# Performance work log

Measured on AMD Instinct MI355X. Metric: run time of the kernel, lower is better.

The kernel has to match this reference:

```python
import jax, jax.numpy as jnp
import numpy as np

N_NODES = 50000
N_EDGES = 1600000
IN_DIM = 128
HID = 64
HEADS = 4
N_GRAPHS = 64
OUT_DIM = 10
NEG_SLOPE = 0.2  # PyG GATConv default leaky_relu slope


def _glorot(key, shape):
    fan_in = shape[0] if len(shape) > 1 else shape[-1]
    return jax.random.normal(key, shape, dtype=jnp.float32) / np.sqrt(fan_in)


def setup_inputs() -> dict:
    key = jax.random.key(0)
    ks = jax.random.split(key, 24)
    imgs = jax.random.normal(ks[0], (N_NODES, IN_DIM), dtype=jnp.float32)
    edge_index = jax.random.randint(ks[1], (2, N_EDGES), 0, N_NODES, dtype=jnp.int32)
    batch = jnp.sort(jax.random.randint(ks[2], (N_NODES,), 0, N_GRAPHS, dtype=jnp.int32))
    HC = HID * HEADS
    inp = {
        'imgs': imgs, 'edge_index': edge_index, 'batch': batch,
        # superpixel aggregator: Linear(input_dim, hidden)
        'W_agg': _glorot(ks[3], (IN_DIM, HID)), 'b_agg': jnp.zeros((HID,), jnp.float32),
        # GAT layer 0: hidden -> heads*hidden, concat
        'W0': _glorot(ks[4], (HID, HC)), 'as0': _glorot(ks[5], (HEADS, HID)), 'ad0': _glorot(ks[6], (HEADS, HID)), 'b0': jnp.zeros((HC,), jnp.float32),
        # GAT layer 1: heads*hidden -> heads*hidden, concat
        'W1': _glorot(ks[7], (HC, HC)), 'as1': _glorot(ks[8], (HEADS, HID)), 'ad1': _glorot(ks[9], (HEADS, HID)), 'b1': jnp.zeros((HC,), jnp.float32),
        # GAT layer 2: heads*hidden -> hidden, mean over heads
        'W2': _glorot(ks[10], (HC, HC)), 'as2': _glorot(ks[11], (HEADS, HID)), 'ad2': _glorot(ks[12], (HEADS, HID)), 'b2': jnp.zeros((HID,), jnp.float32),
        # MLP: hidden -> hidden -> out
        'mW1': _glorot(ks[13], (HID, HID)), 'mb1': jnp.zeros((HID,), jnp.float32),
        'mW2': _glorot(ks[14], (HID, OUT_DIM)), 'mb2': jnp.zeros((OUT_DIM,), jnp.float32),
    }
    return inp


def _gat_conv(x, src, dst, W, a_src, a_dst, b, concat):
    # PyG GATConv: linear -> per-head scores -> leaky_relu -> segment softmax over dst -> scatter-add
    N = x.shape[0]
    H, C = a_src.shape
    h = (x @ W).reshape(N, H, C)                      # [N,H,C]
    es = jnp.sum(h * a_src, axis=-1)                  # [N,H]
    ed = jnp.sum(h * a_dst, axis=-1)                  # [N,H]
    e = jax.nn.leaky_relu(es[src] + ed[dst], NEG_SLOPE)  # [E,H]
    m = jax.ops.segment_max(e, dst, num_segments=N)
    m = jnp.where(jnp.isfinite(m), m, 0.0)
    ex = jnp.exp(e - m[dst])                          # [E,H]
    s = jax.ops.segment_sum(ex, dst, num_segments=N)
    alpha = ex / (s[dst] + 1e-16)                     # [E,H]
    out = jax.ops.segment_sum(h[src] * alpha[..., None], dst, num_segments=N)  # [N,H,C]
    out = out.reshape(N, H * C) if concat else out.mean(axis=1)
    return out + b


def _forward(imgs, edge_index, batch, W_agg, b_agg, W0, as0, ad0, b0, W1, as1, ad1, b1, W2, as2, ad2, b2, mW1, mb1, mW2, mb2):
    N = imgs.shape[0]
    # add self loops (PyG GATConv default add_self_loops=True)
    loop = jnp.arange(N, dtype=edge_index.dtype)
    src = jnp.concatenate([edge_index[0], loop])
    dst = jnp.concatenate([edge_index[1], loop])
    x = imgs @ W_agg + b_agg                          # lrgb aggregator
    x = jax.nn.elu(_gat_conv(x, src, dst, W0, as0, ad0, b0, True))
    x = jax.nn.elu(_gat_conv(x, src, dst, W1, as1, ad1, b1, True))
    x = _gat_conv(x, src, dst, W2, as2, ad2, b2, False)
    # global mean pool over graphs
    sums = jax.ops.segment_sum(x, batch, num_segments=N_GRAPHS)
    cnt = jax.ops.segment_sum(jnp.ones((N,), x.dtype), batch, num_segments=N_GRAPHS)
    pooled = sums / jnp.maximum(cnt, 1.0)[:, None]
    # MLP (dropout inactive at inference)
    hmlp = jax.nn.relu(pooled @ mW1 + mb1)
    return hmlp @ mW2 + mb2


def reference(imgs, edge_index, batch, W_agg, b_agg, W0, as0, ad0, b0, W1, as1, ad1, b1, W2, as2, ad2, b2, mW1, mb1, mW2, mb2):
    return _forward(imgs, edge_index, batch, W_agg, b_agg, W0, as0, ad0, b0, W1, as1, ad1, b1, W2, as2, ad2, b2, mW1, mb1, mW2, mb2)
```

## Files before the change

### kernel.cpp

```cpp
#include <hip/hip_runtime.h>
#include <hip/hip_bf16.h>

#define N_NODES 50000
#define N_EDGESX 1600000
#define E_TOT   (N_EDGESX + N_NODES)
#define IN_DIM 128
#define HID 64
#define HEADS 4
#define HC 256
#define N_GRAPHS 64
#define OUT_DIM 10
#define NEG_SLOPE 0.2f

#define NBUK 196
#define CAP 12288
#define BT 4096

typedef __attribute__((ext_vector_type(8))) short bf16x8;
typedef __attribute__((ext_vector_type(4))) float f32x4;

__device__ __forceinline__ float lrelu(float x){ return fmaxf(x, NEG_SLOPE*x); }
__device__ __forceinline__ float sel4(float4 v, int i){
  float r = v.x;
  r = (i==1) ? v.y : r;
  r = (i==2) ? v.z : r;
  r = (i==3) ? v.w : r;
  return r;
}
__device__ __forceinline__ unsigned short f2bf(float f){
  union { __hip_bfloat16 b; unsigned short u; } cv;
  cv.b = __float2bfloat16(f);
  return cv.u;
}
__device__ __forceinline__ float bf2f(unsigned short u){ return __uint_as_float(((unsigned)u) << 16); }
__device__ __forceinline__ float bflo(unsigned int u){ return __uint_as_float(u << 16); }
__device__ __forceinline__ float bfhi(unsigned int u){ return __uint_as_float(u & 0xffff0000u); }

__global__ __launch_bounds__(256) void bin_k(const int* __restrict__ ei,
                                             int* __restrict__ bucket_cursor,
                                             unsigned int* __restrict__ bucket_buf){
  __shared__ unsigned int pk[BT];
  __shared__ unsigned int binned[BT];
  __shared__ int hist[256], excl[256], gbase[256], lcur[256], tmp[256];
  const int tid = threadIdx.x;
  const int e0 = blockIdx.x * BT;
  const int nv = min(BT, E_TOT - e0);
  hist[tid] = 0;
  __syncthreads();
  for (int i = tid; i < nv; i += 256){
    int e = e0 + i;
    int src, dst;
    if (e < N_EDGESX){ src = ei[e]; dst = ei[N_EDGESX + e]; }
    else { src = e - N_EDGESX; dst = src; }
    pk[i] = ((unsigned)src << 16) | (unsigned)dst;
    atomicAdd(&hist[dst >> 8], 1);
  }
  __syncthreads();
  int v = hist[tid];
  tmp[tid] = v;
  __syncthreads();
  for (int off = 1; off < 256; off <<= 1){
    int t = (tid >= off) ? tmp[tid-off] : 0;
    __syncthreads();
    tmp[tid] += t;
    __syncthreads();
  }
  excl[tid] = tmp[tid] - v;
  lcur[tid] = tmp[tid] - v;
  if (tid < NBUK && v > 0) gbase[tid] = atomicAdd(&bucket_cursor[tid], v);
  __syncthreads();
  for (int i = tid; i < nv; i += 256){
    unsigned u = pk[i];
    int b = (int)((u & 0xFFFFu) >> 8);
    int p = atomicAdd(&lcur[b], 1);
    binned[p] = u;
  }
  __syncthreads();
  for (int j = tid; j < nv; j += 256){
    unsigned u = binned[j];
    int b = (int)((u & 0xFFFFu) >> 8);
    bucket_buf[(size_t)b*CAP + gbase[b] + (j - excl[b])] = u;
  }
}

__global__ __launch_bounds__(256) void bucket_scan_k(const int* __restrict__ bucket_cursor,
                                                     int* __restrict__ bucket_base,
                                                     int* __restrict__ row_start){
  __shared__ int tmp[256];
  int t = threadIdx.x;
  int v = (t < NBUK) ? bucket_cursor[t] : 0;
  tmp[t] = v;
  __syncthreads();
  for (int off = 1; off < 256; off <<= 1){
    int x = (t >= off) ? tmp[t-off] : 0;
    __syncthreads();
    tmp[t] += x;
    __syncthreads();
  }
  if (t < NBUK) bucket_base[t] = tmp[t] - v;
  if (t == 0) row_start[N_NODES] = E_TOT;
}

__global__ __launch_bounds__(256) void build_k(const unsigned int* __restrict__ bucket_buf,
                                               const int* __restrict__ bucket_cursor,
                                               const int* __restrict__ bucket_base,
                                               int* __restrict__ row_start,
                                               int* __restrict__ csr_src){
  __shared__ int hist[256], excl[256], lcur[256], tmp[256];
  const int b = blockIdx.x;
  const int t = threadIdx.x;
  const int cntb = bucket_cursor[b];
  const int base = bucket_base[b];
  const unsigned int* buf = bucket_buf + (size_t)b*CAP;
  hist[t] = 0;
  __syncthreads();
  for (int i = t; i < cntb; i += 256) atomicAdd(&hist[buf[i] & 255], 1);
  __syncthreads();
  int v = hist[t];
  tmp[t] = v;
  __syncthreads();
  for (int off = 1; off < 256; off <<= 1){
    int x = (t >= off) ? tmp[t-off] : 0;
    __syncthreads();
    tmp[t] += x;
    __syncthreads();
  }
  excl[t] = tmp[t] - v;
  lcur[t] = tmp[t] - v;
  int g = b*256 + t;
  if (g < N_NODES) row_start[g] = base + excl[t];
  __syncthreads();
  for (int i = t; i < cntb; i += 256){
    unsigned u = buf[i];
    int p = atomicAdd(&lcur[u & 255], 1);
    csr_src[base + p] = (int)(u >> 16);
  }
}

__global__ __launch_bounds__(256) void wcvt_k(const float* __restrict__ W, unsigned short* __restrict__ WT, int K){
  int idx = blockIdx.x*256 + threadIdx.x;
  if (idx >= K*256) return;
  int k = idx >> 8, c = idx & 255;
  WT[c*K + k] = f2bf(W[k*256 + c]);
}

__global__ __launch_bounds__(256) void wproj_k(const float* __restrict__ W0,
    const float* __restrict__ as0, const float* __restrict__ ad0,
    float* __restrict__ ws0, float* __restrict__ wd0){
  int t = threadIdx.x;
  int h = t >> 6, k = t & 63;
  float s = 0.f, d = 0.f;
  for (int c = 0; c < 64; c++){
    float wv = W0[k*256 + h*64 + c];
    s = fmaf(wv, as0[h*64 + c], s);
    d = fmaf(wv, ad0[h*64 + c], d);
  }
  ws0[t] = s; wd0[t] = d;
}

__global__ __launch_bounds__(256) void agg_lin(const float* __restrict__ imgs, const float* __restrict__ W,
                                               const float* __restrict__ b,
                                               const float* __restrict__ ws0, const float* __restrict__ wd0,
                                               unsigned short* __restrict__ x0,
                                               float* __restrict__ es, float* __restrict__ ed){
  __shared__ __align__(16) float xr[4][IN_DIM];
  int w = threadIdx.x >> 6, lane = threadIdx.x & 63;
  int n = blockIdx.x*4 + w;
  if (n >= N_NODES) return;
  ((float2*)xr[w])[lane] = ((const float2*)(imgs + (size_t)n*IN_DIM))[lane];
  float acc = b[lane];
  #pragma unroll 8
  for (int k = 0; k < IN_DIM; k++)
    acc = fmaf(xr[w][k], W[k*HID + lane], acc);
  x0[(size_t)n*HID + lane] = f2bf(acc);
  float p[4], q[4];
  #pragma unroll
  for (int h = 0; h < 4; h++){
    p[h] = acc * ws0[h*64 + lane];
    q[h] = acc * wd0[h*64 + lane];
  }
  #pragma unroll
  for (int off = 32; off >= 1; off >>= 1){
    #pragma unroll
    for (int h = 0; h < 4; h++){
      p[h] += __shfl_xor(p[h], off);
      q[h] += __shfl_xor(q[h], off);
    }
  }
  if (lane == 0){
    float4 pv; pv.x=p[0]; pv.y=p[1]; pv.z=p[2]; pv.w=p[3];
    float4 qv; qv.x=q[0]; qv.y=q[1]; qv.z=q[2]; qv.w=q[3];
    *(float4*)(es + n*4) = pv;
    *(float4*)(ed + n*4) = qv;
  }
}

__global__ __launch_bounds__(256) void gat_agg0(const unsigned short* __restrict__ x0,
    const float* __restrict__ es, const float* __restrict__ ed,
    const int* __restrict__ row_start, const int* __restrict__ csr_src,
    unsigned short* __restrict__ y4){
  __shared__ int   sbuf[4][64];
  __shared__ float wbuf[4][64][4];
  const int lane = threadIdx.x & 63;
  const int wid  = threadIdx.x >> 6;
  const int n = blockIdx.x*4 + wid;
  if (n >= N_NODES) return;
  const int rs = row_start[n], re = row_start[n+1];
  const float4 edn = *(const float4*)(ed + n*4);
  const int slot = lane >> 3;
  const int f8   = lane & 7;
  float4 sumw = make_float4(0.f,0.f,0.f,0.f);
  float acc[4][8];
  #pragma unroll
  for (int h=0;h<4;h++)
    #pragma unroll
    for (int q2=0;q2<8;q2++) acc[h][q2]=0.f;

  for (int base = rs; base < re; base += 64){
    const int cl = min(64, re - base);
    int e = base + lane;
    int s = (e < re) ? csr_src[e] : 0;
    float4 e4 = *(const float4*)(es + (s<<2));
    float w0 = __expf(lrelu(e4.x + edn.x));
    float w1 = __expf(lrelu(e4.y + edn.y));
    float w2 = __expf(lrelu(e4.z + edn.z));
    float w3 = __expf(lrelu(e4.w + edn.w));
    if (e >= re){ w0=0.f; w1=0.f; w2=0.f; w3=0.f; }
    sumw.x += w0; sumw.y += w1; sumw.z += w2; sumw.w += w3;
    sbuf[wid][lane] = s;
    float4 wv; wv.x=w0; wv.y=w1; wv.z=w2; wv.w=w3;
    *(float4*)wbuf[wid][lane] = wv;
    int j = 0;
    for (; j + 16 <= cl; j += 16){
      int j0 = j + slot, j1 = j + 8 + slot;
      float4 awA = *(const float4*)wbuf[wid][j0]; int sA = sbuf[wid][j0];
      float4 awB = *(const float4*)wbuf[wid][j1]; int sB = sbuf[wid][j1];
      uint4 hvA = *(const uint4*)(x0 + ((unsigned)(sA<<6) + (unsigned)(f8<<3)));
      uint4 hvB = *(const uint4*)(x0 + ((unsigned)(sB<<6) + (unsigned)(f8<<3)));
      float fA[8] = {bflo(hvA.x),bfhi(hvA.x),bflo(hvA.y),bfhi(hvA.y),
                     bflo(hvA.z),bfhi(hvA.z),bflo(hvA.w),bfhi(hvA.w)};
      float fB[8] = {bflo(hvB.x),bfhi(hvB.x),bflo(hvB.y),bfhi(hvB.y),
                     bflo(hvB.z),bfhi(hvB.z),bflo(hvB.w),bfhi(hvB.w)};
      #pragma unroll
      for (int q2=0;q2<8;q2++){
        acc[0][q2] = fmaf(awA.x, fA[q2], acc[0][q2]);
        acc[1][q2] = fmaf(awA.y, fA[q2], acc[1][q2]);
        acc[2][q2] = fmaf(awA.z, fA[q2], acc[2][q2]);
        acc[3][q2] = fmaf(awA.w, fA[q2], acc[3][q2]);
      }
      #pragma unroll
      for (int q2=0;q2<8;q2++){
        acc[0][q2] = fmaf(awB.x, fB[q2], acc[0][q2]);
        acc[1][q2] = fmaf(awB.y, fB[q2], acc[1][q2]);
        acc[2][q2] = fmaf(awB.z, fB[q2], acc[2][q2]);
        acc[3][q2] = fmaf(awB.w, fB[q2], acc[3][q2]);
      }
    }
    for (; j < cl; j += 8){
      int jj = j + slot;
      if (jj < cl){
        float4 aw = *(const float4*)wbuf[wid][jj];
        int s2 = sbuf[wid][jj];
        uint4 hv = *(const uint4*)(x0 + ((unsigned)(s2<<6) + (unsigned)(f8<<3)));
        float f[8] = {bflo(hv.x),bfhi(hv.x),bflo(hv.y),bfhi(hv.y),
                      bflo(hv.z),bfhi(hv.z),bflo(hv.w),bfhi(hv.w)};
        #pragma unroll
        for (int q2=0;q2<8;q2++){
          acc[0][q2] = fmaf(aw.x, f[q2], acc[0][q2]);
          acc[1][q2] = fmaf(aw.y, f[q2], acc[1][q2]);
          acc[2][q2] = fmaf(aw.z, f[q2], acc[2][q2]);
          acc[3][q2] = fmaf(aw.w, f[q2], acc[3][q2]);
        }
      }
    }
  }
  #pragma unroll
  for (int off = 8; off <= 32; off <<= 1){
    #pragma unroll
    for (int h=0;h<4;h++)
      #pragma unroll
      for (int q2=0;q2<8;q2++) acc[h][q2] += __shfl_xor(acc[h][q2], off);
  }
  #pragma unroll
  for (int off = 32; off >= 1; off >>= 1){
    sumw.x += __shfl_xor(sumw.x, off);
    sumw.y += __shfl_xor(sumw.y, off);
    sumw.z += __shfl_xor(sumw.z, off);
    sumw.w += __shfl_xor(sumw.w, off);
  }
  if (lane < 32){
    int h = lane >> 3;
    float inv = 1.f / (sel4(sumw, h) + 1e-16f);
    union { unsigned short u[8]; uint4 v; } ob;
    #pragma unroll
    for (int q2=0;q2<8;q2++) ob.u[q2] = f2bf(acc[h][q2] * inv);
    *(uint4*)(y4 + (size_t)n*HC + lane*8) = ob.v;
  }
}

__global__ __launch_bounds__(256) void hfuse_k(const unsigned short* __restrict__ y4,
                                               const unsigned short* __restrict__ WT0,
                                               const float* __restrict__ b0,
                                               const unsigned short* __restrict__ WT1,
                                               const float* __restrict__ as_, const float* __restrict__ ad_,
                                               unsigned short* __restrict__ h,
                                               float* __restrict__ es, float* __restrict__ ed){
  __shared__ __align__(16) unsigned short xs[16][264];
  __shared__ __align__(16) unsigned short x1s[16][264];
  const int tid = threadIdx.x;
  const int lane = tid & 63;
  const int w = tid >> 6;
  const int n0 = blockIdx.x * 16;
  for (int i = tid; i < 16*32; i += 256){
    int r = i >> 5, cc = (i & 31) * 8;
    *(uint4*)(&xs[r][cc]) = *(const uint4*)(y4 + (size_t)(n0+r)*HC + cc);
  }
  __syncthreads();
  const int g = lane >> 4, cl = lane & 15;
  {
    f32x4 acc[4];
    #pragma unroll
    for (int c = 0; c < 4; c++) acc[c] = (f32x4){0.f,0.f,0.f,0.f};
    #pragma unroll
    for (int t = 0; t < 2; t++){
      bf16x8 a = *(const bf16x8*)(&xs[cl][w*64 + t*32 + g*8]);
      #pragma unroll
      for (int c = 0; c < 4; c++){
        bf16x8 bv = *(const bf16x8*)(WT0 + (size_t)(w*64 + c*16 + cl)*64 + t*32 + g*8);
        acc[c] = __builtin_amdgcn_mfma_f32_16x16x32_bf16(a, bv, acc[c], 0, 0, 0);
      }
    }
    #pragma unroll
    for (int c = 0; c < 4; c++){
      int col = w*64 + c*16 + cl;
      float bb = b0[col];
      #pragma unroll
      for (int j = 0; j < 4; j++){
        float v = acc[c][j] + bb;
        v = v > 0.f ? v : expm1f(v);
        x1s[g*4 + j][col] = f2bf(v);
      }
    }
  }
  __syncthreads();
  f32x4 acc[4];
  #pragma unroll
  for (int c = 0; c < 4; c++) acc[c] = (f32x4){0.f,0.f,0.f,0.f};
  #pragma unroll
  for (int t = 0; t < 8; t++){
    bf16x8 a = *(const bf16x8*)(&x1s[cl][t*32 + g*8]);
    #pragma unroll
    for (int c = 0; c < 4; c++){
      bf16x8 bv = *(const bf16x8*)(WT1 + (size_t)(w*64 + c*16 + cl)*HC + t*32 + g*8);
      acc[c] = __builtin_amdgcn_mfma_f32_16x16x32_bf16(a, bv, acc[c], 0, 0, 0);
    }
  }
  float pes[4] = {0.f,0.f,0.f,0.f}, ped[4] = {0.f,0.f,0.f,0.f};
  #pragma unroll
  for (int c = 0; c < 4; c++){
    float av = as_[w*64 + c*16 + cl];
    float dv = ad_[w*64 + c*16 + cl];
    #pragma unroll
    for (int j = 0; j < 4; j++){
      pes[j] = fmaf(acc[c][j], av, pes[j]);
      ped[j] = fmaf(acc[c][j], dv, ped[j]);
    }
  }
  #pragma unroll
  for (int off = 8; off >= 1; off >>= 1){
    #pragma unroll
    for (int j = 0; j < 4; j++){
      pes[j] += __shfl_xor(pes[j], off);
      ped[j] += __shfl_xor(ped[j], off);
    }
  }
  if (cl == 0){
    #pragma unroll
    for (int j = 0; j < 4; j++){
      int n = n0 + g*4 + j;
      es[n*4 + w] = pes[j];
      ed[n*4 + w] = ped[j];
    }
  }
  #pragma unroll
  for (int c = 0; c < 4; c++){
    #pragma unroll
    for (int j = 0; j < 4; j++){
      h[(size_t)(n0 + g*4 + j)*HC + w*64 + c*16 + cl] = f2bf(acc[c][j]);
    }
  }
}

template<int K>
__global__ __launch_bounds__(256) void lin_mfma(const unsigned short* __restrict__ x,
                                                const unsigned short* __restrict__ WT,
                                                const float* __restrict__ as_, const float* __restrict__ ad_,
                                                unsigned short* __restrict__ h,
                                                float* __restrict__ es, float* __restrict__ ed){
  constexpr int KP = K + 8;
  __shared__ __align__(16) unsigned short xs[16][KP];
  const int tid = threadIdx.x;
  const int lane = tid & 63;
  const int w = tid >> 6;
  const int n0 = blockIdx.x * 16;
  constexpr int CH = K/8;
  for (int i = tid; i < 16*CH; i += 256){
    int r = i / CH, cc = (i % CH)*8;
    *(uint4*)(&xs[r][cc]) = *(const uint4*)(x + (size_t)(n0+r)*K + cc);
  }
  __syncthreads();
  const int g  = lane >> 4;
  const int cl = lane & 15;
  f32x4 acc[4];
  #pragma unroll
  for (int c = 0; c < 4; c++) acc[c] = (f32x4){0.f,0.f,0.f,0.f};
  #pragma unroll
  for (int t = 0; t < K/32; t++){
    bf16x8 a = *(const bf16x8*)(&xs[cl][t*32 + g*8]);
    #pragma unroll
    for (int c = 0; c < 4; c++){
      bf16x8 bv = *(const bf16x8*)(WT + (size_t)(w*64 + c*16 + cl)*K + t*32 + g*8);
      acc[c] = __builtin_amdgcn_mfma_f32_16x16x32_bf16(a, bv, acc[c], 0, 0, 0);
    }
  }
  float pes[4] = {0.f,0.f,0.f,0.f}, ped[4] = {0.f,0.f,0.f,0.f};
  #pragma unroll
  for (int c = 0; c < 4; c++){
    float av = as_[w*64 + c*16 + cl];
    float dv = ad_[w*64 + c*16 + cl];
    #pragma unroll
    for (int j = 0; j < 4; j++){
      pes[j] = fmaf(acc[c][j], av, pes[j]);
      ped[j] = fmaf(acc[c][j], dv, ped[j]);
    }
  }
  #pragma unroll
  for (int off = 8; off >= 1; off >>= 1){
    #pragma unroll
    for (int j = 0; j < 4; j++){
      pes[j] += __shfl_xor(pes[j], off);
      ped[j] += __shfl_xor(ped[j], off);
    }
  }
  if (cl == 0){
    #pragma unroll
    for (int j = 0; j < 4; j++){
      int n = n0 + g*4 + j;
      es[n*4 + w] = pes[j];
      ed[n*4 + w] = ped[j];
    }
  }
  #pragma unroll
  for (int c = 0; c < 4; c++){
    #pragma unroll
    for (int j = 0; j < 4; j++){
      h[(size_t)(n0 + g*4 + j)*HC + w*64 + c*16 + cl] = f2bf(acc[c][j]);
    }
  }
}

template<int ACT>
__global__ __launch_bounds__(256) void gat_agg(const unsigned short* __restrict__ h,
    const float* __restrict__ es, const float* __restrict__ ed,
    const int* __restrict__ row_start, const int* __restrict__ csr_src,
    const float* __restrict__ bias, unsigned short* __restrict__ outp){
  __shared__ int   sbuf[4][64];
  __shared__ float wbuf[4][64][4];
  const int lane = threadIdx.x & 63;
  const int wid  = threadIdx.x >> 6;
  const int n = blockIdx.x*4 + wid;
  if (n >= N_NODES) return;
  const int rs = row_start[n], re = row_start[n+1];
  const float4 edn = *(const float4*)(ed + n*4);
  const int half = lane >> 5;
  const int l5   = lane & 31;
  const int hh   = l5 >> 3;
  const unsigned voff_lane = (unsigned)(l5 << 3);

  float4 sum4 = make_float4(0.f,0.f,0.f,0.f);
  float a0=0.f,a1=0.f,a2=0.f,a3=0.f,a4=0.f,a5=0.f,a6=0.f,a7=0.f;

  for (int base = rs; base < re; base += 64){
    const int cl = min(64, re - base);
    int e = base + lane;
    int s = (e < re) ? csr_src[e] : 0;
    float4 e4 = *(const float4*)(es + (s<<2));
    float w0 = __expf(lrelu(e4.x + edn.x));
    float w1 = __expf(lrelu(e4.y + edn.y));
    float w2 = __expf(lrelu(e4.z + edn.z));
    float w3 = __expf(lrelu(e4.w + edn.w));
    if (e >= re){ w0=0.f; w1=0.f; w2=0.f; w3=0.f; }
    sum4.x += w0; sum4.y += w1; sum4.z += w2; sum4.w += w3;
    sbuf[wid][lane] = s;
    float4 wv4; wv4.x=w0; wv4.y=w1; wv4.z=w2; wv4.w=w3;
    *(float4*)wbuf[wid][lane] = wv4;
    int j = 0;
    for (; j + 4 <= cl; j += 4){
      int j0 = j + half, j1 = j + 2 + half;
      float aA = wbuf[wid][j0][hh]; int sA = sbuf[wid][j0];
      float aB = wbuf[wid][j1][hh]; int sB = sbuf[wid][j1];
      uint4 hA = *(const uint4*)(h + ((unsigned)(sA<<8) + voff_lane));
      uint4 hB = *(const uint4*)(h + ((unsigned)(sB<<8) + voff_lane));
      a0 = fmaf(aA, bflo(hA.x), a0);
      a1 = fmaf(aA, bfhi(hA.x), a1);
      a2 = fmaf(aA, bflo(hA.y), a2);
      a3 = fmaf(aA, bfhi(hA.y), a3);
      a4 = fmaf(aA, bflo(hA.z), a4);
      a5 = fmaf(aA, bfhi(hA.z), a5);
      a6 = fmaf(aA, bflo(hA.w), a6);
      a7 = fmaf(aA, bfhi(hA.w), a7);
      a0 = fmaf(aB, bflo(hB.x), a0);
      a1 = fmaf(aB, bfhi(hB.x), a1);
      a2 = fmaf(aB, bflo(hB.y), a2);
      a3 = fmaf(aB, bfhi(hB.y), a3);
      a4 = fmaf(aB, bflo(hB.z), a4);
      a5 = fmaf(aB, bfhi(hB.z), a5);
      a6 = fmaf(aB, bflo(hB.w), a6);
      a7 = fmaf(aB, bfhi(hB.w), a7);
    }
    for (; j < cl; j += 2){
      int jj = j + half;
      float a  = wbuf[wid][jj][hh];
      int   s2 = sbuf[wid][jj];
      uint4 hv = *(const uint4*)(h + ((unsigned)(s2<<8) + voff_lane));
      a0 = fmaf(a, bflo(hv.x), a0);
      a1 = fmaf(a, bfhi(hv.x), a1);
      a2 = fmaf(a, bflo(hv.y), a2);
      a3 = fmaf(a, bfhi(hv.y), a3);
      a4 = fmaf(a, bflo(hv.z), a4);
      a5 = fmaf(a, bfhi(hv.z), a5);
      a6 = fmaf(a, bflo(hv.w), a6);
      a7 = fmaf(a, bfhi(hv.w), a7);
    }
  }
  #pragma unroll
  for (int off = 32; off >= 1; off >>= 1){
    sum4.x += __shfl_xor(sum4.x, off);
    sum4.y += __shfl_xor(sum4.y, off);
    sum4.z += __shfl_xor(sum4.z, off);
    sum4.w += __shfl_xor(sum4.w, off);
  }
  const float inv = 1.f / (sel4(sum4, hh) + 1e-16f);
  a0 += __shfl_xor(a0, 32); a1 += __shfl_xor(a1, 32);
  a2 += __shfl_xor(a2, 32); a3 += __shfl_xor(a3, 32);
  a4 += __shfl_xor(a4, 32); a5 += __shfl_xor(a5, 32);
  a6 += __shfl_xor(a6, 32); a7 += __shfl_xor(a7, 32);
  float4 o;
  o.x = (half ? a4 : a0) * inv;
  o.y = (half ? a5 : a1) * inv;
  o.z = (half ? a6 : a2) * inv;
  o.w = (half ? a7 : a3) * inv;
  const int fbase = l5*8 + half*4;
  if (ACT){
    float4 b4 = *(const float4*)(bias + fbase);
    o.x += b4.x; o.y += b4.y; o.z += b4.z; o.w += b4.w;
    o.x = o.x > 0.f ? o.x : expm1f(o.x);
    o.y = o.y > 0.f ? o.y : expm1f(o.y);
    o.z = o.z > 0.f ? o.z : expm1f(o.z);
    o.w = o.w > 0.f ? o.w : expm1f(o.w);
  }
  ushort4 ob;
  ob.x = f2bf(o.x); ob.y = f2bf(o.y); ob.z = f2bf(o.z); ob.w = f2bf(o.w);
  *(ushort4*)(outp + (size_t)n*HC + fbase) = ob;
}

#define PB_NODES 128
__global__ __launch_bounds__(256) void pool_k(const unsigned short* __restrict__ xagg,
                                              const int* __restrict__ batch, float* __restrict__ pooled,
                                              float* __restrict__ cnt){
  int c = threadIdx.x & 63;
  int sub = threadIdx.x >> 6;
  int n0 = blockIdx.x * PB_NODES;
  int nend = n0 + PB_NODES; if (nend > N_NODES) nend = N_NODES;
  float acc = 0.f; int curg = -1; int cl = 0;
  for (int n = n0 + sub; n < nend; n += 4){
    int g = batch[n];
    if (g != curg){
      if (curg >= 0){
        unsafeAtomicAdd(pooled + curg*HID + c, acc);
        if (c == 0) unsafeAtomicAdd(cnt + curg, (float)cl);
      }
      curg = g; acc = 0.f; cl = 0;
    }
    const unsigned short* r = xagg + (size_t)n*HC;
    acc += 0.25f*(bf2f(r[c]) + bf2f(r[64+c]) + bf2f(r[128+c]) + bf2f(r[192+c]));
    cl++;
  }
  if (curg >= 0){
    unsafeAtomicAdd(pooled + curg*HID + c, acc);
    if (c == 0) unsafeAtomicAdd(cnt + curg, (float)cl);
  }
}

__global__ __launch_bounds__(64) void mlp_k(const float* __restrict__ pooled, const float* __restrict__ cnt,
                                            const float* __restrict__ b2,
                                            const float* __restrict__ mW1, const float* __restrict__ mb1,
                                            const float* __restrict__ mW2, const float* __restrict__ mb2,
                                            float* __restrict__ out){
  __shared__ float p[HID], h1[HID];
  int g = blockIdx.x, j = threadIdx.x;
  float c = fmaxf(cnt[g], 1.f);
  p[j] = pooled[g*HID + j] / c + b2[j];
  __syncthreads();
  float acc = mb1[j];
  #pragma unroll 8
  for (int k = 0; k < HID; k++) acc = fmaf(p[k], mW1[k*HID + j], acc);
  h1[j] = fmaxf(acc, 0.f);
  __syncthreads();
  if (j < OUT_DIM){
    float a2 = mb2[j];
    #pragma unroll 8
    for (int k = 0; k < HID; k++) a2 = fmaf(h1[k], mW2[k*OUT_DIM + j], a2);
    out[g*OUT_DIM + j] = a2;
  }
}

extern "C" void kernel_launch(void* const* d_in, const int* in_sizes, int n_in,
                              void* d_out, int out_size, void* d_ws, size_t ws_size,
                              hipStream_t stream){
  const float* imgs  = (const float*)d_in[0];
  const int*   ei    = (const int*)d_in[1];
  const int*   batch = (const int*)d_in[2];
  const float* W_agg = (const float*)d_in[3];
  const float* b_agg = (const float*)d_in[4];
  const float* W0 = (const float*)d_in[5];
  const float* as0 = (const float*)d_in[6];
  const float* ad0 = (const float*)d_in[7];
  const float* b0 = (const float*)d_in[8];
  const float* W1 = (const float*)d_in[9];
  const float* as1 = (const float*)d_in[10];
  const float* ad1 = (const float*)d_in[11];
  const float* b1 = (const float*)d_in[12];
  const float* W2 = (const float*)d_in[13];
  const float* as2 = (const float*)d_in[14];
  const float* ad2 = (const float*)d_in[15];
  const float* b2 = (const float*)d_in[16];
  const float* mW1 = (const float*)d_in[17];
  const float* mb1 = (const float*)d_in[18];
  const float* mW2 = (const float*)d_in[19];
  const float* mb2 = (const float*)d_in[20];
  float* out = (float*)d_out;

  unsigned short* y4  = (unsigned short*)d_ws;
  unsigned short* hb  = y4 + (size_t)N_NODES*HC;
  unsigned short* xbf = hb + (size_t)N_NODES*HC;
  float* es   = (float*)(xbf + (size_t)N_NODES*HC);
  float* ed   = es + (size_t)N_NODES*HEADS;
  float* pooled = ed + (size_t)N_NODES*HEADS;
  float* cnt  = pooled + N_GRAPHS*HID;
  float* ws0  = cnt + N_GRAPHS;
  float* wd0  = ws0 + 256;
  int* row_start = (int*)(wd0 + 256);
  int* csr_src   = row_start + (N_NODES+1);
  int* bucket_cursor = csr_src + E_TOT;
  int* bucket_base   = bucket_cursor + NBUK;
  unsigned short* WT0 = (unsigned short*)(bucket_base + NBUK);
  unsigned short* WT1 = WT0 + 256*64;
  unsigned short* WT2 = WT1 + 256*256;
  unsigned int* bucket_buf = (unsigned int*)(WT2 + 256*256);
  unsigned short* x0bf = (unsigned short*)bucket_buf;

  hipMemsetAsync(bucket_cursor, 0, NBUK*sizeof(int), stream);
  bin_k<<<(E_TOT + BT - 1)/BT, 256, 0, stream>>>(ei, bucket_cursor, bucket_buf);
  bucket_scan_k<<<1, 256, 0, stream>>>(bucket_cursor, bucket_base, row_start);
  build_k<<<NBUK, 256, 0, stream>>>(bucket_buf, bucket_cursor, bucket_base, row_start, csr_src);

  wcvt_k<<<(64*256+255)/256, 256, 0, stream>>>(W0, WT0, 64);
  wcvt_k<<<(256*256+255)/256, 256, 0, stream>>>(W1, WT1, 256);
  wcvt_k<<<(256*256+255)/256, 256, 0, stream>>>(W2, WT2, 256);
  wproj_k<<<1, 256, 0, stream>>>(W0, as0, ad0, ws0, wd0);

  const int MB = N_NODES/16;
  const int GB = (N_NODES + 3)/4;

  agg_lin<<<GB, 256, 0, stream>>>(imgs, W_agg, b_agg, ws0, wd0, x0bf, es, ed);

  gat_agg0<<<GB, 256, 0, stream>>>(x0bf, es, ed, row_start, csr_src, y4);

  hfuse_k<<<MB, 256, 0, stream>>>(y4, WT0, b0, WT1, as1, ad1, hb, es, ed);
  gat_agg<1><<<GB, 256, 0, stream>>>(hb, es, ed, row_start, csr_src, b1, xbf);

  lin_mfma<256><<<MB, 256, 0, stream>>>(xbf, WT2, as2, ad2, hb, es, ed);
  gat_agg<0><<<GB, 256, 0, stream>>>(hb, es, ed, row_start, csr_src, nullptr, xbf);

  hipMemsetAsync(pooled, 0, (N_GRAPHS*HID + N_GRAPHS)*sizeof(float), stream);
  pool_k<<<(N_NODES + PB_NODES - 1)/PB_NODES, 256, 0, stream>>>(xbf, batch, pooled, cnt);
  mlp_k<<<N_GRAPHS, 64, 0, stream>>>(pooled, cnt, b2, mW1, mb1, mW2, mb2, out);
}
```

Before: 591.2 us.

## Merge weight prep kernels, unroll gather loop wider, shrink pool tile

After: 596.4 us. About the same (+0.9%).

```diff
diff --git a/kernel.cpp b/kernel.cpp
--- a/kernel.cpp
+++ b/kernel.cpp
@@ -137,25 +137,35 @@
   }
 }
 
-__global__ __launch_bounds__(256) void wcvt_k(const float* __restrict__ W, unsigned short* __restrict__ WT, int K){
-  int idx = blockIdx.x*256 + threadIdx.x;
-  if (idx >= K*256) return;
-  int k = idx >> 8, c = idx & 255;
-  WT[c*K + k] = f2bf(W[k*256 + c]);
-}
-
-__global__ __launch_bounds__(256) void wproj_k(const float* __restrict__ W0,
-    const float* __restrict__ as0, const float* __restrict__ ad0,
-    float* __restrict__ ws0, float* __restrict__ wd0){
-  int t = threadIdx.x;
-  int h = t >> 6, k = t & 63;
-  float s = 0.f, d = 0.f;
-  for (int c = 0; c < 64; c++){
-    float wv = W0[k*256 + h*64 + c];
-    s = fmaf(wv, as0[h*64 + c], s);
-    d = fmaf(wv, ad0[h*64 + c], d);
-  }
-  ws0[t] = s; wd0[t] = d;
+__global__ __launch_bounds__(256) void prep_k(const float* __restrict__ W0, const float* __restrict__ W1,
+                                              const float* __restrict__ W2,
+                                              const float* __restrict__ as0, const float* __restrict__ ad0,
+                                              unsigned short* __restrict__ WT0, unsigned short* __restrict__ WT1,
+                                              unsigned short* __restrict__ WT2,
+                                              float* __restrict__ ws0, float* __restrict__ wd0){
+  const int b = blockIdx.x, t = threadIdx.x;
+  if (b < 64){
+    int idx = b*256 + t;
+    int k = idx >> 8, c = idx & 255;
+    WT0[c*64 + k] = f2bf(W0[k*256 + c]);
+  } else if (b < 320){
+    int idx = (b-64)*256 + t;
+    int k = idx >> 8, c = idx & 255;
+    WT1[c*256 + k] = f2bf(W1[k*256 + c]);
+  } else if (b < 576){
+    int idx = (b-320)*256 + t;
+    int k = idx >> 8, c = idx & 255;
+    WT2[c*256 + k] = f2bf(W2[k*256 + c]);
+  } else {
+    int h = t >> 6, k = t & 63;
+    float s = 0.f, d = 0.f;
+    for (int c = 0; c < 64; c++){
+      float wv = W0[k*256 + h*64 + c];
+      s = fmaf(wv, as0[h*64 + c], s);
+      d = fmaf(wv, ad0[h*64 + c], d);
+    }
+    ws0[t] = s; wd0[t] = d;
+  }
 }
 
 __global__ __launch_bounds__(256) void agg_lin(const float* __restrict__ imgs, const float* __restrict__ W,
@@ -495,42 +505,42 @@
     float4 wv4; wv4.x=w0; wv4.y=w1; wv4.z=w2; wv4.w=w3;
     *(float4*)wbuf[wid][lane] = wv4;
     int j = 0;
-    for (; j + 4 <= cl; j += 4){
-      int j0 = j + half, j1 = j + 2 + half;
+    for (; j + 8 <= cl; j += 8){
+      int j0 = j + half, j1 = j + 2 + half, j2 = j + 4 + half, j3 = j + 6 + half;
       float aA = wbuf[wid][j0][hh]; int sA = sbuf[wid][j0];
       float aB = wbuf[wid][j1][hh]; int sB = sbuf[wid][j1];
+      float aC = wbuf[wid][j2][hh]; int sC = sbuf[wid][j2];
+      float aD = wbuf[wid][j3][hh]; int sD = sbuf[wid][j3];
       uint4 hA = *(const uint4*)(h + ((unsigned)(sA<<8) + voff_lane));
       uint4 hB = *(const uint4*)(h + ((unsigned)(sB<<8) + voff_lane));
-      a0 = fmaf(aA, bflo(hA.x), a0);
-      a1 = fmaf(aA, bfhi(hA.x), a1);
-      a2 = fmaf(aA, bflo(hA.y), a2);
-      a3 = fmaf(aA, bfhi(hA.y), a3);
-      a4 = fmaf(aA, bflo(hA.z), a4);
-      a5 = fmaf(aA, bfhi(hA.z), a5);
-      a6 = fmaf(aA, bflo(hA.w), a6);
-      a7 = fmaf(aA, bfhi(hA.w), a7);
-      a0 = fmaf(aB, bflo(hB.x), a0);
-      a1 = fmaf(aB, bfhi(hB.x), a1);
-      a2 = fmaf(aB, bflo(hB.y), a2);
-      a3 = fmaf(aB, bfhi(hB.y), a3);
-      a4 = fmaf(aB, bflo(hB.z), a4);
-      a5 = fmaf(aB, bfhi(hB.z), a5);
-      a6 = fmaf(aB, bflo(hB.w), a6);
-      a7 = fmaf(aB, bfhi(hB.w), a7);
+      uint4 hC = *(const uint4*)(h + ((unsigned)(sC<<8) + voff_lane));
+      uint4 hD = *(const uint4*)(h + ((unsigned)(sD<<8) + voff_lane));
+      a0 = fmaf(aA, bflo(hA.x), a0); a1 = fmaf(aA, bfhi(hA.x), a1);
+      a2 = fmaf(aA, bflo(hA.y), a2); a3 = fmaf(aA, bfhi(hA.y), a3);
+      a4 = fmaf(aA, bflo(hA.z), a4); a5 = fmaf(aA, bfhi(hA.z), a5);
+      a6 = fmaf(aA, bflo(hA.w), a6); a7 = fmaf(aA, bfhi(hA.w), a7);
+      a0 = fmaf(aB, bflo(hB.x), a0); a1 = fmaf(aB, bfhi(hB.x), a1);
+      a2 = fmaf(aB, bflo(hB.y), a2); a3 = fmaf(aB, bfhi(hB.y), a3);
+      a4 = fmaf(aB, bflo(hB.z), a4); a5 = fmaf(aB, bfhi(hB.z), a5);
+      a6 = fmaf(aB, bflo(hB.w), a6); a7 = fmaf(aB, bfhi(hB.w), a7);
+      a0 = fmaf(aC, bflo(hC.x), a0); a1 = fmaf(aC, bfhi(hC.x), a1);
+      a2 = fmaf(aC, bflo(hC.y), a2); a3 = fmaf(aC, bfhi(hC.y), a3);
+      a4 = fmaf(aC, bflo(hC.z), a4); a5 = fmaf(aC, bfhi(hC.z), a5);
+      a6 = fmaf(aC, bflo(hC.w), a6); a7 = fmaf(aC, bfhi(hC.w), a7);
+      a0 = fmaf(aD, bflo(hD.x), a0); a1 = fmaf(aD, bfhi(hD.x), a1);
+      a2 = fmaf(aD, bflo(hD.y), a2); a3 = fmaf(aD, bfhi(hD.y), a3);
+      a4 = fmaf(aD, bflo(hD.z), a4); a5 = fmaf(aD, bfhi(hD.z), a5);
+      a6 = fmaf(aD, bflo(hD.w), a6); a7 = fmaf(aD, bfhi(hD.w), a7);
     }
     for (; j < cl; j += 2){
       int jj = j + half;
       float a  = wbuf[wid][jj][hh];
       int   s2 = sbuf[wid][jj];
       uint4 hv = *(const uint4*)(h + ((unsigned)(s2<<8) + voff_lane));
-      a0 = fmaf(a, bflo(hv.x), a0);
-      a1 = fmaf(a, bfhi(hv.x), a1);
-      a2 = fmaf(a, bflo(hv.y), a2);
-      a3 = fmaf(a, bfhi(hv.y), a3);
-      a4 = fmaf(a, bflo(hv.z), a4);
-      a5 = fmaf(a, bfhi(hv.z), a5);
-      a6 = fmaf(a, bflo(hv.w), a6);
-      a7 = fmaf(a, bfhi(hv.w), a7);
+      a0 = fmaf(a, bflo(hv.x), a0); a1 = fmaf(a, bfhi(hv.x), a1);
+      a2 = fmaf(a, bflo(hv.y), a2); a3 = fmaf(a, bfhi(hv.y), a3);
+      a4 = fmaf(a, bflo(hv.z), a4); a5 = fmaf(a, bfhi(hv.z), a5);
+      a6 = fmaf(a, bflo(hv.w), a6); a7 = fmaf(a, bfhi(hv.w), a7);
     }
   }
   #pragma unroll
@@ -564,7 +574,7 @@
   *(ushort4*)(outp + (size_t)n*HC + fbase) = ob;
 }
 
-#define PB_NODES 128
+#define PB_NODES 64
 __global__ __launch_bounds__(256) void pool_k(const unsigned short* __restrict__ xagg,
                                               const int* __restrict__ batch, float* __restrict__ pooled,
                                               float* __restrict__ cnt){
@@ -665,10 +675,7 @@
   bucket_scan_k<<<1, 256, 0, stream>>>(bucket_cursor, bucket_base, row_start);
   build_k<<<NBUK, 256, 0, stream>>>(bucket_buf, bucket_cursor, bucket_base, row_start, csr_src);
 
-  wcvt_k<<<(64*256+255)/256, 256, 0, stream>>>(W0, WT0, 64);
-  wcvt_k<<<(256*256+255)/256, 256, 0, stream>>>(W1, WT1, 256);
-  wcvt_k<<<(256*256+255)/256, 256, 0, stream>>>(W2, WT2, 256);
-  wproj_k<<<1, 256, 0, stream>>>(W0, as0, ad0, ws0, wd0);
+  prep_k<<<577, 256, 0, stream>>>(W0, W1, W2, as0, ad0, WT0, WT1, WT2, ws0, wd0);
 
   const int MB = N_NODES/16;
   const int GB = (N_NODES + 3)/4;
```
